# Performance work log

Hardware: AMD Instinct MI355X
Metric: run time of the kernel (lower is better)

Reference implementation:

```python
import jax, jax.numpy as jnp
import numpy as np

D_MODEL = 1024
NHEAD = 16
HEAD_DIM = D_MODEL // NHEAD


def setup_inputs() -> dict:
    key = jax.random.key(0)
    ks = jax.random.split(key, 11)
    B, S = 2, 2048
    s = 1.0 / np.sqrt(D_MODEL)
    return {
        "query": jax.random.normal(ks[0], (B, S, D_MODEL), jnp.float32),
        "key": jax.random.normal(ks[1], (B, S, D_MODEL), jnp.float32),
        "value": jax.random.normal(ks[2], (B, S, D_MODEL), jnp.float32),
        "wq_w": jax.random.normal(ks[3], (D_MODEL, D_MODEL), jnp.float32) * s,
        "wq_b": jax.random.normal(ks[4], (D_MODEL,), jnp.float32) * s,
        "wk_w": jax.random.normal(ks[5], (D_MODEL, D_MODEL), jnp.float32) * s,
        "wk_b": jax.random.normal(ks[6], (D_MODEL,), jnp.float32) * s,
        "wv_w": jax.random.normal(ks[7], (D_MODEL, D_MODEL), jnp.float32) * s,
        "wv_b": jax.random.normal(ks[8], (D_MODEL,), jnp.float32) * s,
        "wo_w": jax.random.normal(ks[9], (D_MODEL, D_MODEL), jnp.float32) * s,
        "wo_b": jax.random.normal(ks[10], (D_MODEL,), jnp.float32) * s,
    }


def reference(query, key, value, wq_w, wq_b, wk_w, wk_b, wv_w, wv_b, wo_w, wo_b):
    B, S, _ = query.shape
    # torch Linear: x @ W.T + b
    def proj(x, w, b):
        y = x @ w.T + b
        return y.reshape(B, S, NHEAD, HEAD_DIM).transpose(0, 2, 1, 3)  # [B,H,S,Dh]

    Q = proj(query, wq_w, wq_b)
    K = proj(key, wk_w, wk_b)
    V = proj(value, wv_w, wv_b)

    scale = 1.0 / np.sqrt(HEAD_DIM).astype(np.float32)
    scores = jnp.einsum("bhqd,bhkd->bhqk", Q, K) * scale  # [B,H,S,S]
    causal = jnp.tril(jnp.ones((S, S), dtype=bool))
    scores = jnp.where(causal, scores, -jnp.inf)
    attn = jax.nn.softmax(scores, axis=-1)
    out = jnp.einsum("bhqk,bhkd->bhqd", attn, V)  # [B,H,S,Dh]
    out = out.transpose(0, 2, 1, 3).reshape(B, S, D_MODEL)
    return out @ wo_w.T + wo_b
```

## Files before the change

kernel.cpp:

```cpp
#include <hip/hip_runtime.h>
#include <stdint.h>

#define D_MODEL 1024
#define S_LEN   2048
#define NHEAD   16
#define HEAD_DIM 64
#define BATCH   2
#define M_TOT   (BATCH * S_LEN)
#define Q_SCALE 0.18033688011112042f

using bf16x8 = __attribute__((ext_vector_type(8))) short;
using f32x4  = __attribute__((ext_vector_type(4))) float;

__device__ __forceinline__ unsigned short f2bf(float f) {
  union { float f; unsigned int u; } v; v.f = f;
  unsigned int u = v.u;
  return (unsigned short)((u + 0x7FFFu + ((u >> 16) & 1u)) >> 16);
}
__device__ __forceinline__ unsigned int pkbf(float a, float b) {
#if __has_builtin(__builtin_amdgcn_cvt_pk_bf16_f32)
  auto p = __builtin_amdgcn_cvt_pk_bf16_f32(a, b);
  union { decltype(p) v; unsigned int u; } c; c.v = p;
  return c.u;
#else
  return (unsigned int)f2bf(a) | ((unsigned int)f2bf(b) << 16);
#endif
}
__device__ __forceinline__ bf16x8 cvt8(const float* p) {
  const float4 a = *(const float4*)p;
  const float4 b = *(const float4*)(p + 4);
  union { unsigned int u[4]; bf16x8 v; } r;
  r.u[0] = pkbf(a.x, a.y); r.u[1] = pkbf(a.z, a.w);
  r.u[2] = pkbf(b.x, b.y); r.u[3] = pkbf(b.z, b.w);
  return r.v;
}
__device__ __forceinline__ float fexp2(float x) {
#if __has_builtin(__builtin_amdgcn_exp2f)
  return __builtin_amdgcn_exp2f(x);
#else
  return __expf(x * 0.69314718055994531f);
#endif
}
__device__ __forceinline__ void async16(const unsigned short* g, short* l) {
  __builtin_amdgcn_global_load_lds(
      reinterpret_cast<const __attribute__((address_space(1))) unsigned int*>(
          reinterpret_cast<uintptr_t>(g)),
      reinterpret_cast<__attribute__((address_space(3))) unsigned int*>(
          reinterpret_cast<uintptr_t>(l)),
      16, 0, 0);
}

__device__ __forceinline__ void swap32(unsigned int& x, unsigned int& y) {
#if __has_builtin(__builtin_amdgcn_permlane32_swap)
  auto r = __builtin_amdgcn_permlane32_swap(x, y, false, false);
  x = (unsigned int)r[0]; y = (unsigned int)r[1];
#else
  const int lane = threadIdx.x & 63;
  unsigned int sx = (unsigned int)__shfl_xor((int)x, 32);
  unsigned int sy = (unsigned int)__shfl_xor((int)y, 32);
  unsigned int nx = (lane & 32) ? sy : x;
  unsigned int ny = (lane & 32) ? y : sx;
  x = nx; y = ny;
#endif
}
__device__ __forceinline__ void swap16(unsigned int& x, unsigned int& y) {
#if __has_builtin(__builtin_amdgcn_permlane16_swap)
  auto r = __builtin_amdgcn_permlane16_swap(x, y, false, false);
  x = (unsigned int)r[0]; y = (unsigned int)r[1];
#else
  const int lane = threadIdx.x & 63;
  unsigned int sx = (unsigned int)__shfl_xor((int)x, 16);
  unsigned int sy = (unsigned int)__shfl_xor((int)y, 16);
  unsigned int nx = (lane & 16) ? sy : x;
  unsigned int ny = (lane & 16) ? y : sx;
  x = nx; y = ny;
#endif
}

#define LDK 40

__global__ __launch_bounds__(256)
void cast_all(const float* __restrict__ wq, const float* __restrict__ wk,
              const float* __restrict__ wv, const float* __restrict__ wo,
              const float* __restrict__ q, const float* __restrict__ k,
              const float* __restrict__ v,
              unsigned short* __restrict__ wb,
              unsigned short* __restrict__ qb, unsigned short* __restrict__ kb,
              unsigned short* __restrict__ vb)
{
  const int z = blockIdx.y;
  const float* src;
  unsigned short* d;
  size_t n;
  switch (z) {
    case 0: src = wq; d = wb;                                   n = (size_t)D_MODEL * D_MODEL; break;
    case 1: src = wk; d = wb + (size_t)1 * D_MODEL * D_MODEL;   n = (size_t)D_MODEL * D_MODEL; break;
    case 2: src = wv; d = wb + (size_t)2 * D_MODEL * D_MODEL;   n = (size_t)D_MODEL * D_MODEL; break;
    case 3: src = wo; d = wb + (size_t)3 * D_MODEL * D_MODEL;   n = (size_t)D_MODEL * D_MODEL; break;
    case 4: src = q;  d = qb;                                   n = (size_t)M_TOT * D_MODEL;   break;
    case 5: src = k;  d = kb;                                   n = (size_t)M_TOT * D_MODEL;   break;
    default: src = v; d = vb;                                   n = (size_t)M_TOT * D_MODEL;   break;
  }
  const size_t i = ((size_t)blockIdx.x * 256 + threadIdx.x) * 8;
  if (i < n) *(bf16x8*)(d + i) = cvt8(src + i);
}

__device__ __forceinline__ void gemm_tile_lds(const unsigned short* __restrict__ A,
                                              const unsigned short* __restrict__ W,
                                              int m0, int n0,
                                              short* As, short* Bs,
                                              f32x4 acc[4][4])
{
  const int t    = threadIdx.x;
  const int lane = t & 63;
  const int w    = t >> 6;
  const int quad = lane >> 4;
  const int l16  = lane & 15;
  const int wm   = (w >> 1) * 64;
  const int wn   = (w & 1) * 64;
  const int srow = w * 16 + (lane >> 2);
  const int scol = (lane & 3) * 8;

  for (int mt = 0; mt < 4; ++mt)
    for (int nt = 0; nt < 4; ++nt)
      acc[mt][nt] = f32x4{0.f, 0.f, 0.f, 0.f};

  for (int kt = 0; kt < D_MODEL / 32; ++kt) {
    const int kc = kt * 32 + scol;
    __syncthreads();
    async16(A + (size_t)(m0 + srow)      * D_MODEL + kc, As + srow * 32 + scol);
    async16(A + (size_t)(m0 + 64 + srow) * D_MODEL + kc, As + (64 + srow) * 32 + scol);
    async16(W + (size_t)(n0 + srow)      * D_MODEL + kc, Bs + srow * 32 + scol);
    async16(W + (size_t)(n0 + 64 + srow) * D_MODEL + kc, Bs + (64 + srow) * 32 + scol);
    __syncthreads();

    bf16x8 af[4], bfr[4];
    for (int mt = 0; mt < 4; ++mt)
      af[mt] = *(const bf16x8*)(As + (wm + mt * 16 + l16) * 32 + quad * 8);
    for (int nt = 0; nt < 4; ++nt)
      bfr[nt] = *(const bf16x8*)(Bs + (wn + nt * 16 + l16) * 32 + quad * 8);
    for (int mt = 0; mt < 4; ++mt)
      for (int nt = 0; nt < 4; ++nt)
        acc[mt][nt] = __builtin_amdgcn_mfma_f32_16x16x32_bf16(af[mt], bfr[nt], acc[mt][nt], 0, 0, 0);
  }
}

__device__ __forceinline__ void gemm_tile_f32(const float* __restrict__ A,
                                              const unsigned short* __restrict__ W,
                                              int m0, int n0,
                                              short* As, short* Bs,
                                              f32x4 acc[4][4])
{
  const int t    = threadIdx.x;
  const int lane = t & 63;
  const int w    = t >> 6;
  const int quad = lane >> 4;
  const int l16  = lane & 15;
  const int wm   = (w >> 1) * 64;
  const int wn   = (w & 1) * 64;
  const int srow = t >> 2;
  const int scol = (t & 3) * 8;

  for (int mt = 0; mt < 4; ++mt)
    for (int nt = 0; nt < 4; ++nt)
      acc[mt][nt] = f32x4{0.f, 0.f, 0.f, 0.f};

  for (int kt = 0; kt < D_MODEL / 32; ++kt) {
    const int kc = kt * 32 + scol;
    const bf16x8 a0 = cvt8(A + (size_t)(m0 + srow)      * D_MODEL + kc);
    const bf16x8 a1 = cvt8(A + (size_t)(m0 + srow + 64) * D_MODEL + kc);
    const bf16x8 b0 = *(const bf16x8*)(W + (size_t)(n0 + srow)      * D_MODEL + kc);
    const bf16x8 b1 = *(const bf16x8*)(W + (size_t)(n0 + srow + 64) * D_MODEL + kc);
    __syncthreads();
    *(bf16x8*)(As + (srow)      * LDK + scol) = a0;
    *(bf16x8*)(As + (srow + 64) * LDK + scol) = a1;
    *(bf16x8*)(Bs + (srow)      * LDK + scol) = b0;
    *(bf16x8*)(Bs + (srow + 64) * LDK + scol) = b1;
    __syncthreads();

    bf16x8 af[4], bfr[4];
    for (int mt = 0; mt < 4; ++mt)
      af[mt] = *(const bf16x8*)(As + (wm + mt * 16 + l16) * LDK + quad * 8);
    for (int nt = 0; nt < 4; ++nt)
      bfr[nt] = *(const bf16x8*)(Bs + (wn + nt * 16 + l16) * LDK + quad * 8);
    for (int mt = 0; mt < 4; ++mt)
      for (int nt = 0; nt < 4; ++nt)
        acc[mt][nt] = __builtin_amdgcn_mfma_f32_16x16x32_bf16(af[mt], bfr[nt], acc[mt][nt], 0, 0, 0);
  }
}

__device__ __forceinline__ void qkv_epilogue(int z, int m0, int n0,
                                             const float* __restrict__ bias,
                                             float scale,
                                             unsigned short* __restrict__ dst,
                                             f32x4 acc[4][4])
{
  const int t    = threadIdx.x;
  const int lane = t & 63;
  const int w    = t >> 6;
  const int quad = lane >> 4;
  const int l16  = lane & 15;
  const int wm   = (w >> 1) * 64;
  const int wn   = (w & 1) * 64;

  for (int nt = 0; nt < 4; ++nt) {
    const int n = n0 + wn + nt * 16 + l16;
    const float bb = bias[n];
    const int h = n >> 6, d = n & 63;
    for (int mt = 0; mt < 4; ++mt) {
      for (int r = 0; r < 4; ++r) {
        const int m = m0 + wm + mt * 16 + quad * 4 + r;
        const int b = m >> 11, s = m & 2047;
        const unsigned short val = f2bf((acc[mt][nt][r] + bb) * scale);
        if (z < 2)
          dst[((size_t)((b * NHEAD + h) * S_LEN + s)) * HEAD_DIM + d] = val;
        else
          dst[((size_t)((b * NHEAD + h) * HEAD_DIM + d)) * S_LEN + s] = val;
      }
    }
  }
}

__global__ __launch_bounds__(256)
void qkv_fast(const unsigned short* __restrict__ qb,
              const unsigned short* __restrict__ kb,
              const unsigned short* __restrict__ vb,
              const unsigned short* __restrict__ wqb,
              const unsigned short* __restrict__ wkb,
              const unsigned short* __restrict__ wvb,
              const float* __restrict__ bq, const float* __restrict__ bk,
              const float* __restrict__ bv,
              unsigned short* __restrict__ Qh, unsigned short* __restrict__ Kh,
              unsigned short* __restrict__ VhT)
{
  __shared__ __attribute__((aligned(16))) short As[128 * 32];
  __shared__ __attribute__((aligned(16))) short Bs[128 * 32];
  const int z = blockIdx.z;
  const unsigned short* A    = (z == 0) ? qb  : (z == 1) ? kb  : vb;
  const unsigned short* W    = (z == 0) ? wqb : (z == 1) ? wkb : wvb;
  const float*          bias = (z == 0) ? bq  : (z == 1) ? bk  : bv;
  unsigned short*       dst  = (z == 0) ? Qh  : (z == 1) ? Kh  : VhT;
  const float           scale = (z == 0) ? Q_SCALE : 1.0f;

  const int m0 = blockIdx.x * 128, n0 = blockIdx.y * 128;
  f32x4 acc[4][4];
  gemm_tile_lds(A, W, m0, n0, As, Bs, acc);
  qkv_epilogue(z, m0, n0, bias, scale, dst, acc);
}

__global__ __launch_bounds__(256)
void qkv_slow(const float* __restrict__ query, const float* __restrict__ key,
              const float* __restrict__ value,
              const unsigned short* __restrict__ wqb,
              const unsigned short* __restrict__ wkb,
              const unsigned short* __restrict__ wvb,
              const float* __restrict__ bq, const float* __restrict__ bk,
              const float* __restrict__ bv,
              unsigned short* __restrict__ Qh, unsigned short* __restrict__ Kh,
              unsigned short* __restrict__ VhT)
{
  __shared__ __attribute__((aligned(16))) short As[128 * LDK];
  __shared__ __attribute__((aligned(16))) short Bs[128 * LDK];
  const int z = blockIdx.z;
  const float*          A    = (z == 0) ? query : (z == 1) ? key : value;
  const unsigned short* W    = (z == 0) ? wqb   : (z == 1) ? wkb : wvb;
  const float*          bias = (z == 0) ? bq    : (z == 1) ? bk  : bv;
  unsigned short*       dst  = (z == 0) ? Qh    : (z == 1) ? Kh  : VhT;
  const float           scale = (z == 0) ? Q_SCALE : 1.0f;

  const int m0 = blockIdx.x * 128, n0 = blockIdx.y * 128;
  f32x4 acc[4][4];
  gemm_tile_f32(A, W, m0, n0, As, Bs, acc);
  qkv_epilogue(z, m0, n0, bias, scale, dst, acc);
}

__global__ __launch_bounds__(256)
void out_proj(const unsigned short* __restrict__ Oh,
              const unsigned short* __restrict__ wob,
              const float* __restrict__ bo,
              float* __restrict__ dst)
{
  __shared__ __attribute__((aligned(16))) short As[128 * 32];
  __shared__ __attribute__((aligned(16))) short Bs[128 * 32];
  const int m0 = blockIdx.x * 128, n0 = blockIdx.y * 128;
  f32x4 acc[4][4];
  gemm_tile_lds(Oh, wob, m0, n0, As, Bs, acc);

  const int t    = threadIdx.x;
  const int lane = t & 63;
  const int w    = t >> 6;
  const int quad = lane >> 4;
  const int l16  = lane & 15;
  const int wm   = (w >> 1) * 64;
  const int wn   = (w & 1) * 64;

  for (int nt = 0; nt < 4; ++nt) {
    const int n = n0 + wn + nt * 16 + l16;
    const float bb = bo[n];
    for (int mt = 0; mt < 4; ++mt)
      for (int r = 0; r < 4; ++r) {
        const int m = m0 + wm + mt * 16 + quad * 4 + r;
        dst[(size_t)m * D_MODEL + n] = acc[mt][nt][r] + bb;
      }
  }
}

struct Frags { bf16x8 ka0, ka1, kb0, kb1, v0, v1, v2, v3; };
struct StageRegs { bf16x8 k0, k1, k2, k3, v0, v1, v2, v3; };

#define KS_LD 72
#define VT_LD 136

__device__ __forceinline__ StageRegs load_stage(const unsigned short* __restrict__ Kb,
                                                const unsigned short* __restrict__ Vb,
                                                int k0, int kr, int kc, int vd, int vc) {
  StageRegs r;
  r.k0 = *(const bf16x8*)(Kb + (size_t)(k0 + kr)      * HEAD_DIM + kc);
  r.k1 = *(const bf16x8*)(Kb + (size_t)(k0 + kr + 32) * HEAD_DIM + kc);
  r.k2 = *(const bf16x8*)(Kb + (size_t)(k0 + kr + 64) * HEAD_DIM + kc);
  r.k3 = *(const bf16x8*)(Kb + (size_t)(k0 + kr + 96) * HEAD_DIM + kc);
  r.v0 = *(const bf16x8*)(Vb + (size_t)(vd)      * S_LEN + k0 + vc);
  r.v1 = *(const bf16x8*)(Vb + (size_t)(vd + 16) * S_LEN + k0 + vc);
  r.v2 = *(const bf16x8*)(Vb + (size_t)(vd + 32) * S_LEN + k0 + vc);
  r.v3 = *(const bf16x8*)(Vb + (size_t)(vd + 48) * S_LEN + k0 + vc);
  return r;
}
__device__ __forceinline__ void write_stage(const StageRegs& r, short* Ks, short* Vts,
                                            int kr, int kc, int vd, int vc) {
  *(bf16x8*)(Ks + (kr)      * KS_LD + kc) = r.k0;
  *(bf16x8*)(Ks + (kr + 32) * KS_LD + kc) = r.k1;
  *(bf16x8*)(Ks + (kr + 64) * KS_LD + kc) = r.k2;
  *(bf16x8*)(Ks + (kr + 96) * KS_LD + kc) = r.k3;
  *(bf16x8*)(Vts + (vd)      * VT_LD + vc) = r.v0;
  *(bf16x8*)(Vts + (vd + 16) * VT_LD + vc) = r.v1;
  *(bf16x8*)(Vts + (vd + 32) * VT_LD + vc) = r.v2;
  *(bf16x8*)(Vts + (vd + 48) * VT_LD + vc) = r.v3;
}
__device__ __forceinline__ Frags lds_frags(const short* Ks, const short* Vts,
                                           int c, int quad, int l16) {
  Frags f;
  const short* kp = Ks + (c * 32 + l16) * KS_LD + quad * 8;
  f.ka0 = *(const bf16x8*)(kp);
  f.ka1 = *(const bf16x8*)(kp + 32);
  f.kb0 = *(const bf16x8*)(kp + 16 * KS_LD);
  f.kb1 = *(const bf16x8*)(kp + 16 * KS_LD + 32);
  const short* vp = Vts + l16 * VT_LD + c * 32 + quad * 8;
  f.v0 = *(const bf16x8*)(vp);
  f.v1 = *(const bf16x8*)(vp + 16 * VT_LD);
  f.v2 = *(const bf16x8*)(vp + 32 * VT_LD);
  f.v3 = *(const bf16x8*)(vp + 48 * VT_LD);
  return f;
}

template <bool DIAG>
__device__ __forceinline__ void proc_chunk(const Frags& f, const bf16x8 qf[2][2],
                                           const bf16x8& ones, int quad, int l16,
                                           f32x4 lacc[2], f32x4 oacc[2][4]) {
  f32x4 sA0 = f32x4{0.f, 0.f, 0.f, 0.f};
  f32x4 sA1 = f32x4{0.f, 0.f, 0.f, 0.f};
  f32x4 sB0 = f32x4{0.f, 0.f, 0.f, 0.f};
  f32x4 sB1 = f32x4{0.f, 0.f, 0.f, 0.f};
  sA0 = __builtin_amdgcn_mfma_f32_16x16x32_bf16(f.ka0, qf[0][0], sA0, 0, 0, 0);
  sA0 = __builtin_amdgcn_mfma_f32_16x16x32_bf16(f.ka1, qf[0][1], sA0, 0, 0, 0);
  sA1 = __builtin_amdgcn_mfma_f32_16x16x32_bf16(f.ka0, qf[1][0], sA1, 0, 0, 0);
  sA1 = __builtin_amdgcn_mfma_f32_16x16x32_bf16(f.ka1, qf[1][1], sA1, 0, 0, 0);
  if (!DIAG) {
    sB0 = __builtin_amdgcn_mfma_f32_16x16x32_bf16(f.kb0, qf[0][0], sB0, 0, 0, 0);
    sB0 = __builtin_amdgcn_mfma_f32_16x16x32_bf16(f.kb1, qf[0][1], sB0, 0, 0, 0);
  }
  sB1 = __builtin_amdgcn_mfma_f32_16x16x32_bf16(f.kb0, qf[1][0], sB1, 0, 0, 0);
  sB1 = __builtin_amdgcn_mfma_f32_16x16x32_bf16(f.kb1, qf[1][1], sB1, 0, 0, 0);

  float stA0[4], stB0[4], stA1[4], stB1[4];
  const int kl = quad * 4;
#pragma unroll
  for (int r = 0; r < 4; ++r) {
    if (!DIAG) {
      stA0[r] = fexp2(sA0[r]);
      stB0[r] = fexp2(sB0[r]);
      stB1[r] = fexp2(sB1[r]);
    } else {
      stA0[r] = (kl + r <= l16) ? fexp2(sA0[r]) : 0.f;
      stB0[r] = 0.f;
      stB1[r] = (kl + r <= l16) ? fexp2(sB1[r]) : 0.f;
    }
    stA1[r] = fexp2(sA1[r]);
  }

  unsigned int a0 = pkbf(stA0[0], stA0[1]), b0 = pkbf(stA0[2], stA0[3]);
  unsigned int c0_ = pkbf(stB0[0], stB0[1]), e0 = pkbf(stB0[2], stB0[3]);
  swap32(a0, c0_); swap32(b0, e0);
  swap16(a0, c0_); swap16(b0, e0);
  union { unsigned int u[4]; bf16x8 v; } p0;
  p0.u[0] = a0; p0.u[1] = b0; p0.u[2] = c0_; p0.u[3] = e0;
  unsigned int a1 = pkbf(stA1[0], stA1[1]), b1 = pkbf(stA1[2], stA1[3]);
  unsigned int c1_ = pkbf(stB1[0], stB1[1]), e1 = pkbf(stB1[2], stB1[3]);
  swap32(a1, c1_); swap32(b1, e1);
  swap16(a1, c1_); swap16(b1, e1);
  union { unsigned int u[4]; bf16x8 v; } p1;
  p1.u[0] = a1; p1.u[1] = b1; p1.u[2] = c1_; p1.u[3] = e1;

  lacc[0] = __builtin_amdgcn_mfma_f32_16x16x32_bf16(p0.v, ones, lacc[0], 0, 0, 0);
  lacc[1] = __builtin_amdgcn_mfma_f32_16x16x32_bf16(p1.v, ones, lacc[1], 0, 0, 0);
  oacc[0][0] = __builtin_amdgcn_mfma_f32_16x16x32_bf16(p0.v, f.v0, oacc[0][0], 0, 0, 0);
  oacc[1][0] = __builtin_amdgcn_mfma_f32_16x16x32_bf16(p1.v, f.v0, oacc[1][0], 0, 0, 0);
  oacc[0][1] = __builtin_amdgcn_mfma_f32_16x16x32_bf16(p0.v, f.v1, oacc[0][1], 0, 0, 0);
  oacc[1][1] = __builtin_amdgcn_mfma_f32_16x16x32_bf16(p1.v, f.v1, oacc[1][1], 0, 0, 0);
  oacc[0][2] = __builtin_amdgcn_mfma_f32_16x16x32_bf16(p0.v, f.v2, oacc[0][2], 0, 0, 0);
  oacc[1][2] = __builtin_amdgcn_mfma_f32_16x16x32_bf16(p1.v, f.v2, oacc[1][2], 0, 0, 0);
  oacc[0][3] = __builtin_amdgcn_mfma_f32_16x16x32_bf16(p0.v, f.v3, oacc[0][3], 0, 0, 0);
  oacc[1][3] = __builtin_amdgcn_mfma_f32_16x16x32_bf16(p1.v, f.v3, oacc[1][3], 0, 0, 0);
}

__global__ __launch_bounds__(256)
void attn_kernel(const unsigned short* __restrict__ Qh,
                 const unsigned short* __restrict__ Kh,
                 const unsigned short* __restrict__ VhT,
                 unsigned short* __restrict__ O)
{
  __shared__ __attribute__((aligned(16))) short Ks[128 * KS_LD];
  __shared__ __attribute__((aligned(16))) short Vts[64 * VT_LD];

  const int orig = blockIdx.x;
  const int xcd  = orig & 7;
  const int li   = orig >> 3;
  const int bh   = xcd * 4 + (li & 3);
  const int qt   = 15 - (li >> 2);
  const int q0   = qt * 128;
  const int b    = bh >> 4;
  const int h    = bh & 15;
  const int t    = threadIdx.x;
  const int w    = t >> 6;
  const int lane = t & 63;
  const int quad = lane >> 4;
  const int l16  = lane & 15;
  const int rowbase = q0 + w * 32;

  const unsigned short* Kb = Kh + (size_t)bh * S_LEN * HEAD_DIM;
  const unsigned short* Vb = VhT + (size_t)bh * HEAD_DIM * S_LEN;
  const int kr = t >> 3, kc = (t & 7) * 8;
  const int vd = t >> 4, vc = (t & 15) * 8;

  bf16x8 qf[2][2];
#pragma unroll
  for (int mt = 0; mt < 2; ++mt) {
    const size_t qrow = (size_t)bh * S_LEN + rowbase + mt * 16 + l16;
    qf[mt][0] = *(const bf16x8*)(Qh + qrow * HEAD_DIM + quad * 8);
    qf[mt][1] = *(const bf16x8*)(Qh + qrow * HEAD_DIM + 32 + quad * 8);
  }
  bf16x8 ones;
#pragma unroll
  for (int j = 0; j < 8; ++j) ones[j] = (short)0x3F80;

  f32x4 lacc[2];
  f32x4 oacc[2][4];
  lacc[0] = f32x4{0.f, 0.f, 0.f, 0.f};
  lacc[1] = f32x4{0.f, 0.f, 0.f, 0.f};
#pragma unroll
  for (int mt = 0; mt < 2; ++mt)
#pragma unroll
    for (int dt = 0; dt < 4; ++dt) oacc[mt][dt] = f32x4{0.f, 0.f, 0.f, 0.f};

  const int nT = qt + 1;
  StageRegs rs = load_stage(Kb, Vb, 0, kr, kc, vd, vc);
  for (int j = 0; j < nT; ++j) {
    __syncthreads();
    write_stage(rs, Ks, Vts, kr, kc, vd, vc);
    __syncthreads();
    if (j + 1 < nT) rs = load_stage(Kb, Vb, (j + 1) * 128, kr, kc, vd, vc);
    if (j < qt) {
#pragma unroll
      for (int c = 0; c < 4; ++c) {
        const Frags f = lds_frags(Ks, Vts, c, quad, l16);
        proc_chunk<false>(f, qf, ones, quad, l16, lacc, oacc);
      }
    } else {
      for (int c = 0; c < w; ++c) {
        const Frags f = lds_frags(Ks, Vts, c, quad, l16);
        proc_chunk<false>(f, qf, ones, quad, l16, lacc, oacc);
      }
      const Frags f = lds_frags(Ks, Vts, w, quad, l16);
      proc_chunk<true>(f, qf, ones, quad, l16, lacc, oacc);
    }
  }

#pragma unroll
  for (int mt = 0; mt < 2; ++mt)
#pragma unroll
    for (int dt = 0; dt < 4; ++dt)
#pragma unroll
      for (int r = 0; r < 4; ++r) {
        const int rowg = rowbase + mt * 16 + quad * 4 + r;
        O[(size_t)(b * S_LEN + rowg) * D_MODEL + h * 64 + dt * 16 + l16] =
            f2bf(oacc[mt][dt][r] / lacc[mt][r]);
      }
}

extern "C" void kernel_launch(void* const* d_in, const int* in_sizes, int n_in,
                              void* d_out, int out_size, void* d_ws, size_t ws_size,
                              hipStream_t stream)
{
  (void)in_sizes; (void)n_in; (void)out_size;
  const float* q  = (const float*)d_in[0];
  const float* k  = (const float*)d_in[1];
  const float* v  = (const float*)d_in[2];
  const float* wq = (const float*)d_in[3];
  const float* bq = (const float*)d_in[4];
  const float* wk = (const float*)d_in[5];
  const float* bk = (const float*)d_in[6];
  const float* wv = (const float*)d_in[7];
  const float* bv = (const float*)d_in[8];
  const float* wo = (const float*)d_in[9];
  const float* bo = (const float*)d_in[10];
  float* out = (float*)d_out;

  unsigned short* wb  = (unsigned short*)d_ws;
  unsigned short* wqb = wb;
  unsigned short* wkb = wb + (size_t)1 * D_MODEL * D_MODEL;
  unsigned short* wvb = wb + (size_t)2 * D_MODEL * D_MODEL;
  unsigned short* wob = wb + (size_t)3 * D_MODEL * D_MODEL;
  unsigned short* Kh  = wb + (size_t)4 * D_MODEL * D_MODEL;
  unsigned short* VhT = Kh + (size_t)M_TOT * D_MODEL;
  unsigned short* Oh  = VhT + (size_t)M_TOT * D_MODEL;
  unsigned short* qb  = Oh;
  unsigned short* vb  = Oh + (size_t)M_TOT * D_MODEL;
  unsigned short* Qh  = (unsigned short*)d_out;
  unsigned short* kb  = Qh + (size_t)M_TOT * D_MODEL;

  const bool fast = ws_size >= (size_t)40 * 1024 * 1024;

  dim3 g1(M_TOT / 128, D_MODEL / 128, 3);
  if (fast) {
    dim3 gc((size_t)M_TOT * D_MODEL / (256 * 8), 7, 1);
    cast_all<<<gc, 256, 0, stream>>>(wq, wk, wv, wo, q, k, v, wb, qb, kb, vb);
    qkv_fast<<<g1, 256, 0, stream>>>(qb, kb, vb, wqb, wkb, wvb, bq, bk, bv, Qh, Kh, VhT);
  } else {
    dim3 gc((size_t)D_MODEL * D_MODEL / (256 * 8), 4, 1);
    cast_all<<<gc, 256, 0, stream>>>(wq, wk, wv, wo, q, k, v, wb, qb, kb, vb);
    qkv_slow<<<g1, 256, 0, stream>>>(q, k, v, wqb, wkb, wvb, bq, bk, bv, Qh, Kh, VhT);
  }

  dim3 g2(512, 1, 1);
  attn_kernel<<<g2, 256, 0, stream>>>(Qh, Kh, VhT, Oh);

  dim3 g3(M_TOT / 128, D_MODEL / 128, 1);
  out_proj<<<g3, 256, 0, stream>>>(Oh, wob, bo, out);
}
```

Measured before the change: 217.1 us.

## Widen GEMM K-tile with XOR-swizzled LDS, double-buffer attention K/V, add MFMA priority

The shared GEMM tile loop now stages 64-wide K slices (twice the LDS) with an XOR swizzle on the column index, halving the number of barrier pairs and reducing LDS bank conflicts on fragment reads. The attention kernel gains ping-pong LDS buffers for K and V, so the next tile is written after compute with one barrier per iteration instead of two. s_setprio is raised around the MFMA bursts in proc_chunk to favour matrix-issue waves. The larger LDS footprint may lower occupancy in both the GEMM and attention kernels.

```diff
diff --git a/kernel.cpp b/kernel.cpp
--- a/kernel.cpp
+++ b/kernel.cpp
@@ -118,30 +118,45 @@
   const int l16  = lane & 15;
   const int wm   = (w >> 1) * 64;
   const int wn   = (w & 1) * 64;
-  const int srow = w * 16 + (lane >> 2);
-  const int scol = (lane & 3) * 8;
+  const int srow = t >> 3;
+  const int sc   = t & 7;
+  const int scg  = (sc ^ (srow & 7)) * 8;
+  const int sdst = srow * 64 + sc * 8;
+  const int rk   = l16 & 7;
 
   for (int mt = 0; mt < 4; ++mt)
     for (int nt = 0; nt < 4; ++nt)
       acc[mt][nt] = f32x4{0.f, 0.f, 0.f, 0.f};
 
-  for (int kt = 0; kt < D_MODEL / 32; ++kt) {
-    const int kc = kt * 32 + scol;
+  for (int kt = 0; kt < D_MODEL / 64; ++kt) {
+    const int kc = kt * 64 + scg;
     __syncthreads();
-    async16(A + (size_t)(m0 + srow)      * D_MODEL + kc, As + srow * 32 + scol);
-    async16(A + (size_t)(m0 + 64 + srow) * D_MODEL + kc, As + (64 + srow) * 32 + scol);
-    async16(W + (size_t)(n0 + srow)      * D_MODEL + kc, Bs + srow * 32 + scol);
-    async16(W + (size_t)(n0 + 64 + srow) * D_MODEL + kc, Bs + (64 + srow) * 32 + scol);
+    async16(A + (size_t)(m0 + srow)      * D_MODEL + kc, As + sdst);
+    async16(A + (size_t)(m0 + 32 + srow) * D_MODEL + kc, As + sdst + 32 * 64);
+    async16(A + (size_t)(m0 + 64 + srow) * D_MODEL + kc, As + sdst + 64 * 64);
+    async16(A + (size_t)(m0 + 96 + srow) * D_MODEL + kc, As + sdst + 96 * 64);
+    async16(W + (size_t)(n0 + srow)      * D_MODEL + kc, Bs + sdst);
+    async16(W + (size_t)(n0 + 32 + srow) * D_MODEL + kc, Bs + sdst + 32 * 64);
+    async16(W + (size_t)(n0 + 64 + srow) * D_MODEL + kc, Bs + sdst + 64 * 64);
+    async16(W + (size_t)(n0 + 96 + srow) * D_MODEL + kc, Bs + sdst + 96 * 64);
     __syncthreads();
 
-    bf16x8 af[4], bfr[4];
-    for (int mt = 0; mt < 4; ++mt)
-      af[mt] = *(const bf16x8*)(As + (wm + mt * 16 + l16) * 32 + quad * 8);
-    for (int nt = 0; nt < 4; ++nt)
-      bfr[nt] = *(const bf16x8*)(Bs + (wn + nt * 16 + l16) * 32 + quad * 8);
-    for (int mt = 0; mt < 4; ++mt)
+#pragma unroll
+    for (int ks = 0; ks < 2; ++ks) {
+      const int cidx = ((ks * 4 + quad) ^ rk) * 8;
+      bf16x8 af[4], bfr[4];
+#pragma unroll
+      for (int mt = 0; mt < 4; ++mt)
+        af[mt] = *(const bf16x8*)(As + (wm + mt * 16 + l16) * 64 + cidx);
+#pragma unroll
       for (int nt = 0; nt < 4; ++nt)
-        acc[mt][nt] = __builtin_amdgcn_mfma_f32_16x16x32_bf16(af[mt], bfr[nt], acc[mt][nt], 0, 0, 0);
+        bfr[nt] = *(const bf16x8*)(Bs + (wn + nt * 16 + l16) * 64 + cidx);
+#pragma unroll
+      for (int mt = 0; mt < 4; ++mt)
+#pragma unroll
+        for (int nt = 0; nt < 4; ++nt)
+          acc[mt][nt] = __builtin_amdgcn_mfma_f32_16x16x32_bf16(af[mt], bfr[nt], acc[mt][nt], 0, 0, 0);
+    }
   }
 }
 
@@ -233,8 +248,8 @@
               unsigned short* __restrict__ Qh, unsigned short* __restrict__ Kh,
               unsigned short* __restrict__ VhT)
 {
-  __shared__ __attribute__((aligned(16))) short As[128 * 32];
-  __shared__ __attribute__((aligned(16))) short Bs[128 * 32];
+  __shared__ __attribute__((aligned(16))) short As[128 * 64];
+  __shared__ __attribute__((aligned(16))) short Bs[128 * 64];
   const int z = blockIdx.z;
   const unsigned short* A    = (z == 0) ? qb  : (z == 1) ? kb  : vb;
   const unsigned short* W    = (z == 0) ? wqb : (z == 1) ? wkb : wvb;
@@ -280,8 +295,8 @@
               const float* __restrict__ bo,
               float* __restrict__ dst)
 {
-  __shared__ __attribute__((aligned(16))) short As[128 * 32];
-  __shared__ __attribute__((aligned(16))) short Bs[128 * 32];
+  __shared__ __attribute__((aligned(16))) short As[128 * 64];
+  __shared__ __attribute__((aligned(16))) short Bs[128 * 64];
   const int m0 = blockIdx.x * 128, n0 = blockIdx.y * 128;
   f32x4 acc[4][4];
   gemm_tile_lds(Oh, wob, m0, n0, As, Bs, acc);
@@ -360,6 +375,7 @@
   f32x4 sA1 = f32x4{0.f, 0.f, 0.f, 0.f};
   f32x4 sB0 = f32x4{0.f, 0.f, 0.f, 0.f};
   f32x4 sB1 = f32x4{0.f, 0.f, 0.f, 0.f};
+  __builtin_amdgcn_s_setprio(1);
   sA0 = __builtin_amdgcn_mfma_f32_16x16x32_bf16(f.ka0, qf[0][0], sA0, 0, 0, 0);
   sA0 = __builtin_amdgcn_mfma_f32_16x16x32_bf16(f.ka1, qf[0][1], sA0, 0, 0, 0);
   sA1 = __builtin_amdgcn_mfma_f32_16x16x32_bf16(f.ka0, qf[1][0], sA1, 0, 0, 0);
@@ -370,6 +386,7 @@
   }
   sB1 = __builtin_amdgcn_mfma_f32_16x16x32_bf16(f.kb0, qf[1][0], sB1, 0, 0, 0);
   sB1 = __builtin_amdgcn_mfma_f32_16x16x32_bf16(f.kb1, qf[1][1], sB1, 0, 0, 0);
+  __builtin_amdgcn_s_setprio(0);
 
   float stA0[4], stB0[4], stA1[4], stB1[4];
   const int kl = quad * 4;
@@ -400,6 +417,7 @@
   union { unsigned int u[4]; bf16x8 v; } p1;
   p1.u[0] = a1; p1.u[1] = b1; p1.u[2] = c1_; p1.u[3] = e1;
 
+  __builtin_amdgcn_s_setprio(1);
   lacc[0] = __builtin_amdgcn_mfma_f32_16x16x32_bf16(p0.v, ones, lacc[0], 0, 0, 0);
   lacc[1] = __builtin_amdgcn_mfma_f32_16x16x32_bf16(p1.v, ones, lacc[1], 0, 0, 0);
   oacc[0][0] = __builtin_amdgcn_mfma_f32_16x16x32_bf16(p0.v, f.v0, oacc[0][0], 0, 0, 0);
@@ -410,6 +428,7 @@
   oacc[1][2] = __builtin_amdgcn_mfma_f32_16x16x32_bf16(p1.v, f.v2, oacc[1][2], 0, 0, 0);
   oacc[0][3] = __builtin_amdgcn_mfma_f32_16x16x32_bf16(p0.v, f.v3, oacc[0][3], 0, 0, 0);
   oacc[1][3] = __builtin_amdgcn_mfma_f32_16x16x32_bf16(p1.v, f.v3, oacc[1][3], 0, 0, 0);
+  __builtin_amdgcn_s_setprio(0);
 }
 
 __global__ __launch_bounds__(256)
@@ -418,8 +437,8 @@
                  const unsigned short* __restrict__ VhT,
                  unsigned short* __restrict__ O)
 {
-  __shared__ __attribute__((aligned(16))) short Ks[128 * KS_LD];
-  __shared__ __attribute__((aligned(16))) short Vts[64 * VT_LD];
+  __shared__ __attribute__((aligned(16))) short Ks[2][128 * KS_LD];
+  __shared__ __attribute__((aligned(16))) short Vts[2][64 * VT_LD];
 
   const int orig = blockIdx.x;
   const int xcd  = orig & 7;
@@ -463,25 +482,31 @@
 
   const int nT = qt + 1;
   StageRegs rs = load_stage(Kb, Vb, 0, kr, kc, vd, vc);
+  write_stage(rs, Ks[0], Vts[0], kr, kc, vd, vc);
+  __syncthreads();
   for (int j = 0; j < nT; ++j) {
-    __syncthreads();
-    write_stage(rs, Ks, Vts, kr, kc, vd, vc);
-    __syncthreads();
-    if (j + 1 < nT) rs = load_stage(Kb, Vb, (j + 1) * 128, kr, kc, vd, vc);
+    const short* Ksj = (j & 1) ? Ks[1] : Ks[0];
+    const short* Vtj = (j & 1) ? Vts[1] : Vts[0];
+    short* Ksn = (j & 1) ? Ks[0] : Ks[1];
+    short* Vtn = (j & 1) ? Vts[0] : Vts[1];
+    const bool more = (j + 1 < nT);
+    if (more) rs = load_stage(Kb, Vb, (j + 1) * 128, kr, kc, vd, vc);
     if (j < qt) {
 #pragma unroll
       for (int c = 0; c < 4; ++c) {
-        const Frags f = lds_frags(Ks, Vts, c, quad, l16);
+        const Frags f = lds_frags(Ksj, Vtj, c, quad, l16);
         proc_chunk<false>(f, qf, ones, quad, l16, lacc, oacc);
       }
     } else {
       for (int c = 0; c < w; ++c) {
-        const Frags f = lds_frags(Ks, Vts, c, quad, l16);
+        const Frags f = lds_frags(Ksj, Vtj, c, quad, l16);
         proc_chunk<false>(f, qf, ones, quad, l16, lacc, oacc);
       }
-      const Frags f = lds_frags(Ks, Vts, w, quad, l16);
+      const Frags f = lds_frags(Ksj, Vtj, w, quad, l16);
       proc_chunk<true>(f, qf, ones, quad, l16, lacc, oacc);
     }
+    if (more) write_stage(rs, Ksn, Vtn, kr, kc, vd, vc);
+    __syncthreads();
   }
 
 #pragma unroll
```

New measurement: 228.2 us. +5.1%, slower.
